# Kernel tuning notes

Measured on AMD Instinct MI355X. Metric: run time of the kernel, lower is better.

## Reference

```python
import jax, jax.numpy as jnp
import numpy as np

N = 50000
E = 800000
HID = 128


def _gat_conv(x, src, dst, W, al, ar, b, n):
    # DGL GATConv, num_heads=1, negative_slope=0.2, bias=True
    z = x @ W                                  # [N, F]
    el = z @ al                                # [N]
    er = z @ ar                                # [N]
    e = jax.nn.leaky_relu(el[src] + er[dst], 0.2)   # [E]
    m = jax.ops.segment_max(e, dst, num_segments=n)  # per-dst max for stable softmax
    ex = jnp.exp(e - m[dst])
    denom = jax.ops.segment_sum(ex, dst, num_segments=n)
    alpha = ex / (denom[dst] + 1e-9)           # edge softmax over incoming edges
    out = jax.ops.segment_sum(alpha[:, None] * z[src], dst, num_segments=n)
    return out + b


def setup_inputs() -> dict:
    key = jax.random.key(0)
    ks = jax.random.split(key, 16)
    inp = {
        "x": jax.random.normal(ks[0], (N, 2), jnp.float32),
        "src": jax.random.randint(ks[1], (E,), 0, N, jnp.int32),
        "dst": jax.random.randint(ks[2], (E,), 0, N, jnp.int32),
        "W1": jax.random.normal(ks[3], (2, HID), jnp.float32) * 0.5,
        "al1": jax.random.normal(ks[4], (HID,), jnp.float32) * 0.1,
        "ar1": jax.random.normal(ks[5], (HID,), jnp.float32) * 0.1,
        "b1": jnp.zeros((HID,), jnp.float32),
        "W2": jax.random.normal(ks[6], (HID, HID), jnp.float32) * (1.0 / np.sqrt(HID)),
        "al2": jax.random.normal(ks[7], (HID,), jnp.float32) * 0.1,
        "ar2": jax.random.normal(ks[8], (HID,), jnp.float32) * 0.1,
        "b2": jnp.zeros((HID,), jnp.float32),
        "Wlin": jax.random.normal(ks[9], (HID, 3), jnp.float32) * (1.0 / np.sqrt(HID)),
        "blin": jnp.zeros((3,), jnp.float32),
        "alpha0": jnp.float32(1.0),
        "beta0": jnp.float32(1.0),
        "gamma0": jnp.float32(1.0),
        "dt": jnp.float32(0.5),
    }
    return inp


def reference(x, src, dst, W1, al1, ar1, b1, W2, al2, ar2, b2, Wlin, blin,
              alpha0, beta0, gamma0, dt):
    h = _gat_conv(x, src, dst, W1, al1, ar1, b1, N)
    h = jax.nn.relu(h)
    h = _gat_conv(h, src, dst, W2, al2, ar2, b2, N)
    h = jax.nn.relu(h)
    h = jax.nn.sigmoid(h @ Wlin + blin)        # [N, 3]
    # (original computes unsplice/splice predictions from alpha0/beta0/gamma0/dt
    #  but does not return them; returned value is the mean over rate channels)
    return h.mean(axis=-1)                     # [N]


if __name__ == "__main__":
    out = reference(**setup_inputs())
    print(out.shape, out.dtype)
```

## Files before the change

### kernel.cpp

```cpp
#include <hip/hip_runtime.h>
#include <math.h>

#define NN 50000
#define EE 800000
#define HIDF 128
#define NPAD 50176

#define BSHIFT 9
#define BKTN 98
#define BCAP 10000

typedef unsigned int uint;
typedef unsigned short ushort;
typedef unsigned char uchar;
typedef short bf16x8 __attribute__((ext_vector_type(8)));
typedef float f32x4 __attribute__((ext_vector_type(4)));

__device__ inline ushort bf16_rtne(float x) {
  uint u = __float_as_uint(x);
  return (ushort)((u + 0x7fffu + ((u >> 16) & 1u)) >> 16);
}
__device__ inline uint pack2_bf16(float a, float b) {
  return (uint)bf16_rtne(a) | ((uint)bf16_rtne(b) << 16);
}
__device__ inline float rdlanef(float p, int jj) {
  return __uint_as_float(__builtin_amdgcn_readlane(__float_as_uint(p), jj));
}

__global__ void k_prep(const float* __restrict__ x, const float* __restrict__ W1,
                       const float* __restrict__ al1, const float* __restrict__ ar1,
                       const float* __restrict__ W2, const float* __restrict__ al2,
                       const float* __restrict__ ar2,
                       ushort* __restrict__ z, float* __restrict__ el, float* __restrict__ er,
                       ushort* __restrict__ Bfrag, float* __restrict__ wel,
                       float* __restrict__ wer, int* __restrict__ bcnt) {
  int b = blockIdx.x, tid = threadIdx.x;
  if (b < 16) {
    int e = b * 1024 + tid * 4;
#pragma unroll
    for (int q = 0; q < 4; ++q, ++e) {
      int k = e >> 7, n = e & 127;
      float v = W2[e];
      ushort hi = bf16_rtne(v);
      ushort lo = bf16_rtne(v - __uint_as_float((uint)hi << 16));
      int g = n >> 4, t = k >> 5;
      int l = (n & 15) | (((k >> 3) & 3) << 4);
      int j = k & 7;
      int idx = ((g * 4 + t) * 64 + l) * 8 + j;
      Bfrag[idx] = hi;
      Bfrag[16384 + idx] = lo;
    }
  } else if (b == 16) {
    if (tid < BKTN) bcnt[tid] = 0;
    if (tid < 128) {
      float acc = 0.f;
      for (int k = 0; k < 128; ++k) acc += W2[k * 128 + tid] * al2[k];
      wel[tid] = acc;
    } else {
      int n = tid - 128;
      float acc = 0.f;
      for (int k = 0; k < 128; ++k) acc += W2[k * 128 + n] * ar2[k];
      wer[n] = acc;
    }
  } else {
    int v = (b - 17) * 4 + (tid >> 6);
    if (v >= NN) return;
    int lane = tid & 63;
    float x0 = x[v * 2 + 0];
    float x1 = x[v * 2 + 1];
    int f0 = lane * 2, f1 = f0 + 1;
    float z0 = fmaf(x0, W1[f0], x1 * W1[HIDF + f0]);
    float z1v = fmaf(x0, W1[f1], x1 * W1[HIDF + f1]);
    ((uint*)(z + (size_t)v * HIDF))[lane] = pack2_bf16(z0, z1v);
    float elp = z0 * al1[f0] + z1v * al1[f1];
    float erp = z0 * ar1[f0] + z1v * ar1[f1];
    for (int o = 32; o; o >>= 1) {
      elp += __shfl_xor(elp, o);
      erp += __shfl_xor(erp, o);
    }
    if (lane == 0) { el[v] = elp; er[v] = erp; }
  }
}

__global__ __launch_bounds__(256) void k_binA(const int* __restrict__ src,
                                              const int* __restrict__ dst,
                                              int* __restrict__ bcnt, uint* __restrict__ bcoo) {
  __shared__ uint stage[4096];
  __shared__ uchar stageb[4096];
  __shared__ int bh[BKTN], bbase[BKTN], gbase[BKTN], lcur[BKTN];
  __shared__ int sc[128];
  int tid = threadIdx.x;
  int e0 = blockIdx.x * 4096;
  int nE = min(4096, EE - e0);
  if (tid < BKTN) bh[tid] = 0;
  __syncthreads();

  int myb[16];
  uint myv[16];
#pragma unroll
  for (int k = 0; k < 16; ++k) {
    int i = e0 + k * 256 + tid;
    myb[k] = -1;
    if (i < EE) {
      int s = src[i], d = dst[i];
      myb[k] = d >> BSHIFT;
      myv[k] = ((uint)s << BSHIFT) | (uint)(d & 511);
      atomicAdd(&bh[myb[k]], 1);
    }
  }
  __syncthreads();

  {
    int v = (tid < BKTN) ? bh[tid] : 0;
    if (tid < 128) sc[tid] = v;
    __syncthreads();
    for (int o = 1; o < 128; o <<= 1) {
      int add = (tid >= o && tid < 128) ? sc[tid - o] : 0;
      __syncthreads();
      if (tid < 128) sc[tid] += add;
      __syncthreads();
    }
    if (tid < BKTN) {
      int excl = sc[tid] - bh[tid];
      bbase[tid] = excl;
      lcur[tid] = excl;
      gbase[tid] = atomicAdd(&bcnt[tid], bh[tid]);
    }
  }
  __syncthreads();

#pragma unroll
  for (int k = 0; k < 16; ++k) {
    if (myb[k] >= 0) {
      int slot = atomicAdd(&lcur[myb[k]], 1);
      stage[slot] = myv[k];
      stageb[slot] = (uchar)myb[k];
    }
  }
  __syncthreads();

  for (int s2 = tid; s2 < nE; s2 += 256) {
    int b = stageb[s2];
    bcoo[(size_t)b * BCAP + gbase[b] + (s2 - bbase[b])] = stage[s2];
  }
}

__global__ __launch_bounds__(256) void k_binB(const uint* __restrict__ bcoo,
                                              const int* __restrict__ bcnt,
                                              int* __restrict__ rowp, int* __restrict__ srcs) {
  __shared__ int h[512], pref[512], ps[256];
  __shared__ int basebuf;
  int b = blockIdx.x, tid = threadIdx.x;
  int cnt = bcnt[b];

  {
    int v = (tid < BKTN) ? bcnt[tid] : 0;
    if (tid < 128) ps[tid] = v;
    __syncthreads();
    for (int o = 1; o < 128; o <<= 1) {
      int add = (tid >= o && tid < 128) ? ps[tid - o] : 0;
      __syncthreads();
      if (tid < 128) ps[tid] += add;
      __syncthreads();
    }
    if (tid == 0) {
      basebuf = (b == 0) ? 0 : ps[b - 1];
      if (b == 0) rowp[NN] = EE;
    }
  }
  h[tid] = 0;
  h[tid + 256] = 0;
  __syncthreads();
  int base = basebuf;
  const uint* mc = bcoo + (size_t)b * BCAP;
  for (int i = tid; i < cnt; i += 256) atomicAdd(&h[mc[i] & 511], 1);
  __syncthreads();
  int a0 = h[2 * tid], a1 = h[2 * tid + 1];
  int s = a0 + a1;
  ps[tid] = s;
  __syncthreads();
  for (int o = 1; o < 256; o <<= 1) {
    int add = (tid >= o) ? ps[tid - o] : 0;
    __syncthreads();
    ps[tid] += add;
    __syncthreads();
  }
  int excl = ps[tid] - s;
  pref[2 * tid] = excl;
  pref[2 * tid + 1] = excl + a0;
  __syncthreads();
  int n0 = b << BSHIFT;
  for (int j = tid; j < 512; j += 256)
    if (n0 + j < NN) rowp[n0 + j] = base + pref[j];
  __syncthreads();
  for (int i = tid; i < cnt; i += 256) {
    uint v = mc[i];
    int pos = atomicAdd(&pref[v & 511], 1);
    srcs[base + pos] = (int)(v >> BSHIFT);
  }
}

__global__ __launch_bounds__(256) void k_gemm_mfma(
    const ushort* __restrict__ Hhi, const ushort* __restrict__ Hlo,
    const ushort* __restrict__ Bfrag, ushort* __restrict__ z) {
  int tid = threadIdx.x;
  int lane = tid & 63;
  int wid = tid >> 6;
  int base = blockIdx.x * 128;

  bf16x8 bhi[2][4], blo[2][4];
  const bf16x8* bp = (const bf16x8*)Bfrag;
#pragma unroll
  for (int gi = 0; gi < 2; ++gi)
#pragma unroll
    for (int t = 0; t < 4; ++t) {
      int idx = ((wid * 2 + gi) * 4 + t) * 64 + lane;
      bhi[gi][t] = bp[idx];
      blo[gi][t] = bp[2048 + idx];
    }

  int arow = lane & 15;
  int koff = (lane >> 4) * 8;
  const bf16x8* ahp = (const bf16x8*)(Hhi + (size_t)(base + arow) * HIDF + koff);
  const bf16x8* alp = (const bf16x8*)(Hlo + (size_t)(base + arow) * HIDF + koff);

  bf16x8 ah[4], av[4];
#pragma unroll
  for (int t = 0; t < 4; ++t) { ah[t] = ahp[t * 4]; av[t] = alp[t * 4]; }

#pragma unroll
  for (int mt = 0; mt < 8; ++mt) {
    bf16x8 nah[4], nav[4];
#pragma unroll
    for (int t = 0; t < 4; ++t) { nah[t] = ah[t]; nav[t] = av[t]; }
    if (mt < 7) {
#pragma unroll
      for (int t = 0; t < 4; ++t) {
        nah[t] = ahp[(mt + 1) * 256 + t * 4];
        nav[t] = alp[(mt + 1) * 256 + t * 4];
      }
    }
    f32x4 c0a = {0.f, 0.f, 0.f, 0.f}, c0b = {0.f, 0.f, 0.f, 0.f};
    f32x4 c1a = {0.f, 0.f, 0.f, 0.f}, c1b = {0.f, 0.f, 0.f, 0.f};
#pragma unroll
    for (int t = 0; t < 4; ++t) {
      f32x4& c0 = (t & 1) ? c0b : c0a;
      f32x4& c1 = (t & 1) ? c1b : c1a;
      c0 = __builtin_amdgcn_mfma_f32_16x16x32_bf16(ah[t], bhi[0][t], c0, 0, 0, 0);
      c1 = __builtin_amdgcn_mfma_f32_16x16x32_bf16(ah[t], bhi[1][t], c1, 0, 0, 0);
      c0 = __builtin_amdgcn_mfma_f32_16x16x32_bf16(ah[t], blo[0][t], c0, 0, 0, 0);
      c1 = __builtin_amdgcn_mfma_f32_16x16x32_bf16(ah[t], blo[1][t], c1, 0, 0, 0);
      c0 = __builtin_amdgcn_mfma_f32_16x16x32_bf16(av[t], bhi[0][t], c0, 0, 0, 0);
      c1 = __builtin_amdgcn_mfma_f32_16x16x32_bf16(av[t], bhi[1][t], c1, 0, 0, 0);
    }
    f32x4 c0 = c0a + c0b;
    f32x4 c1 = c1a + c1b;
    int r0 = base + mt * 16 + (lane >> 4) * 4;
    int cc = wid * 32 + (lane & 15);
    ushort* zp = z + (size_t)r0 * HIDF + cc;
#pragma unroll
    for (int i = 0; i < 4; ++i) {
      zp[i * HIDF] = bf16_rtne(c0[i]);
      zp[i * HIDF + 16] = bf16_rtne(c1[i]);
    }
#pragma unroll
    for (int t = 0; t < 4; ++t) { ah[t] = nah[t]; av[t] = nav[t]; }
  }
}

#define PAIR(JJ)                                                        \
  {                                                                     \
    float pA = rdlanef(p, (JJ)), pB = rdlanef(p, (JJ) + 1);             \
    int sA = __builtin_amdgcn_readlane(s, (JJ));                        \
    int sB = __builtin_amdgcn_readlane(s, (JJ) + 1);                    \
    uint zA = zw[(uint)sA * 64u + (uint)lane];                          \
    uint zB = zw[(uint)sB * 64u + (uint)lane];                          \
    ax = fmaf(pA, __uint_as_float(zA << 16), ax);                       \
    ay = fmaf(pA, __uint_as_float(zA & 0xffff0000u), ay);               \
    ax = fmaf(pB, __uint_as_float(zB << 16), ax);                       \
    ay = fmaf(pB, __uint_as_float(zB & 0xffff0000u), ay);               \
  }

template <int MODE>
__global__ void k_aggregate(const int* __restrict__ rowp, const int* __restrict__ srcs,
                            const float* __restrict__ el, const float* __restrict__ er,
                            const ushort* __restrict__ z, const float* __restrict__ bias,
                            ushort* __restrict__ Hhi, ushort* __restrict__ Hlo,
                            const float* __restrict__ wel, const float* __restrict__ wer,
                            float* __restrict__ elo, float* __restrict__ ero,
                            float* __restrict__ out,
                            const float* __restrict__ Wlin, const float* __restrict__ blin) {
  int v = blockIdx.x * 4 + (threadIdx.x >> 6);
  if (v >= NN) return;
  int lane = threadIdx.x & 63;
  int beg = rowp[v], end = rowp[v + 1];
  float erv = er[v];
  float psum = 0.f;
  float ax = 0.f, ay = 0.f;
  const uint* zw = (const uint*)z;

  for (int cb = beg; cb < end; cb += 64) {
    int j = cb + lane;
    bool valid = j < end;
    int s = srcs[valid ? j : beg];
    float t = el[s] + erv;
    t = fmaxf(t, 0.2f * t);
    float p = valid ? __expf(t) : 0.f;
    psum += p;
    int cnt = min(64, end - cb);
    int bb = 0;
    for (; bb + 16 <= cnt; bb += 16) {
#pragma unroll
      for (int u = 0; u < 16; u += 2) PAIR(bb + u)
    }
    for (; bb < cnt; bb += 2) PAIR(bb)
  }

  float denom = psum;
  for (int o = 32; o; o >>= 1) denom += __shfl_xor(denom, o);
  float inv = 1.0f / (denom + 1e-9f);
  float2 bv = ((const float2*)bias)[lane];
  float ox = fmaxf(fmaf(ax, inv, bv.x), 0.f);
  float oy = fmaxf(fmaf(ay, inv, bv.y), 0.f);

  if (MODE == 1) {
    ushort hx = bf16_rtne(ox), hy = bf16_rtne(oy);
    ((uint*)Hhi)[(size_t)v * 64 + lane] = (uint)hx | ((uint)hy << 16);
    float lx = ox - __uint_as_float((uint)hx << 16);
    float ly = oy - __uint_as_float((uint)hy << 16);
    ((uint*)Hlo)[(size_t)v * 64 + lane] = pack2_bf16(lx, ly);
    float2 wl = ((const float2*)wel)[lane];
    float2 wr = ((const float2*)wer)[lane];
    float ep = ox * wl.x + oy * wl.y;
    float rp = ox * wr.x + oy * wr.y;
    for (int o = 32; o; o >>= 1) {
      ep += __shfl_xor(ep, o);
      rp += __shfl_xor(rp, o);
    }
    if (lane == 0) { elo[v] = ep; ero[v] = rp; }
  } else {
    int f0 = lane * 2;
    const float* w0 = &Wlin[f0 * 3];
    float d0 = fmaf(ox, w0[0], oy * w0[3]);
    float d1 = fmaf(ox, w0[1], oy * w0[4]);
    float d2 = fmaf(ox, w0[2], oy * w0[5]);
    for (int o = 32; o; o >>= 1) {
      d0 += __shfl_xor(d0, o);
      d1 += __shfl_xor(d1, o);
      d2 += __shfl_xor(d2, o);
    }
    if (lane == 0) {
      float s0 = 1.f / (1.f + __expf(-(d0 + blin[0])));
      float s1 = 1.f / (1.f + __expf(-(d1 + blin[1])));
      float s2 = 1.f / (1.f + __expf(-(d2 + blin[2])));
      out[v] = (s0 + s1 + s2) * (1.f / 3.f);
    }
  }
}

extern "C" void kernel_launch(void* const* d_in, const int* in_sizes, int n_in,
                              void* d_out, int out_size, void* d_ws, size_t ws_size,
                              hipStream_t stream) {
  const float* x    = (const float*)d_in[0];
  const int*   src  = (const int*)d_in[1];
  const int*   dst  = (const int*)d_in[2];
  const float* W1   = (const float*)d_in[3];
  const float* al1  = (const float*)d_in[4];
  const float* ar1  = (const float*)d_in[5];
  const float* b1   = (const float*)d_in[6];
  const float* W2   = (const float*)d_in[7];
  const float* al2  = (const float*)d_in[8];
  const float* ar2  = (const float*)d_in[9];
  const float* b2   = (const float*)d_in[10];
  const float* Wlin = (const float*)d_in[11];
  const float* blin = (const float*)d_in[12];
  float* out = (float*)d_out;

  char* ws = (char*)d_ws;
  size_t off = 0;
  auto alloc = [&](size_t bytes) -> char* {
    char* p = ws + off;
    off += (bytes + 255) & ~(size_t)255;
    return p;
  };
  int*    rowp    = (int*)alloc((size_t)(NN + 1) * 4);
  int*    srcs    = (int*)alloc((size_t)EE * 4);
  int*    bcnt    = (int*)alloc(BKTN * 4);
  uint*   bcoo    = (uint*)alloc((size_t)BKTN * BCAP * 4);
  float*  el1     = (float*)alloc((size_t)NN * 4);
  float*  er1     = (float*)alloc((size_t)NN * 4);
  float*  el2     = (float*)alloc((size_t)NN * 4);
  float*  er2     = (float*)alloc((size_t)NN * 4);
  float*  wel     = (float*)alloc(HIDF * 4);
  float*  wer     = (float*)alloc(HIDF * 4);
  ushort* Bfrag   = (ushort*)alloc(2 * 16384 * 2);
  ushort* Z       = (ushort*)alloc((size_t)NPAD * HIDF * 2);
  ushort* Hhi     = (ushort*)alloc((size_t)NPAD * HIDF * 2);
  ushort* Hlo     = (ushort*)alloc((size_t)NPAD * HIDF * 2);

  const int nbNode4 = (NN + 3) / 4;
  const int nbGemm = (NN + 127) / 128;
  const int nbBinA = (EE + 4095) / 4096;

  k_prep<<<17 + nbNode4, 256, 0, stream>>>(x, W1, al1, ar1, W2, al2, ar2,
                                           Z, el1, er1, Bfrag, wel, wer, bcnt);

  k_binA<<<nbBinA, 256, 0, stream>>>(src, dst, bcnt, bcoo);
  k_binB<<<BKTN, 256, 0, stream>>>(bcoo, bcnt, rowp, srcs);

  k_aggregate<1><<<nbNode4, 256, 0, stream>>>(rowp, srcs, el1, er1, Z, b1,
                                              Hhi, Hlo, wel, wer, el2, er2,
                                              nullptr, nullptr, nullptr);

  k_gemm_mfma<<<nbGemm, 256, 0, stream>>>(Hhi, Hlo, Bfrag, Z);
  k_aggregate<2><<<nbNode4, 256, 0, stream>>>(rowp, srcs, el2, er2, Z, b2,
                                              nullptr, nullptr, nullptr, nullptr, nullptr, nullptr,
                                              out, Wlin, blin);
}
```

Measured before the change: 146.3 us.

## Precompute edge exp weights and split aggregation across feature quarters

Adds a per-edge kernel that computes the exponentiated attention logit once and packs it with the source index. Aggregation now launches four blocks per node group, each handling a 32-feature quarter, with four edge subgroups per wave. Partial el2/er2 and final linear outputs are accumulated with atomics, and a separate finalize kernel applies the sigmoid. This raises parallelism and removes readlane serialization, but it adds extra kernels, recomputes the softmax denominator in every quarter, adds atomics, and writes an 8-byte-per-edge array.

```diff
diff --git a/kernel.cpp b/kernel.cpp
--- a/kernel.cpp
+++ b/kernel.cpp
@@ -23,9 +23,8 @@
 __device__ inline uint pack2_bf16(float a, float b) {
   return (uint)bf16_rtne(a) | ((uint)bf16_rtne(b) << 16);
 }
-__device__ inline float rdlanef(float p, int jj) {
-  return __uint_as_float(__builtin_amdgcn_readlane(__float_as_uint(p), jj));
-}
+__device__ inline float lo16(uint z) { return __uint_as_float(z << 16); }
+__device__ inline float hi16(uint z) { return __uint_as_float(z & 0xffff0000u); }
 
 __global__ void k_prep(const float* __restrict__ x, const float* __restrict__ W1,
                        const float* __restrict__ al1, const float* __restrict__ ar1,
@@ -33,7 +32,9 @@
                        const float* __restrict__ ar2,
                        ushort* __restrict__ z, float* __restrict__ el, float* __restrict__ er,
                        ushort* __restrict__ Bfrag, float* __restrict__ wel,
-                       float* __restrict__ wer, int* __restrict__ bcnt) {
+                       float* __restrict__ wer, int* __restrict__ bcnt,
+                       float* __restrict__ el2, float* __restrict__ er2,
+                       float* __restrict__ out3) {
   int b = blockIdx.x, tid = threadIdx.x;
   if (b < 16) {
     int e = b * 1024 + tid * 4;
@@ -78,7 +79,11 @@
       elp += __shfl_xor(elp, o);
       erp += __shfl_xor(erp, o);
     }
-    if (lane == 0) { el[v] = elp; er[v] = erp; }
+    if (lane == 0) {
+      el[v] = elp; er[v] = erp;
+      el2[v] = 0.f; er2[v] = 0.f;
+      out3[v] = 0.f; out3[NN + v] = 0.f; out3[2 * NN + v] = 0.f;
+    }
   }
 }
 
@@ -147,7 +152,8 @@
 
 __global__ __launch_bounds__(256) void k_binB(const uint* __restrict__ bcoo,
                                               const int* __restrict__ bcnt,
-                                              int* __restrict__ rowp, int* __restrict__ srcs) {
+                                              int* __restrict__ rowp, int* __restrict__ srcs,
+                                              int* __restrict__ dstc) {
   __shared__ int h[512], pref[512], ps[256];
   __shared__ int basebuf;
   int b = blockIdx.x, tid = threadIdx.x;
@@ -197,7 +203,19 @@
     uint v = mc[i];
     int pos = atomicAdd(&pref[v & 511], 1);
     srcs[base + pos] = (int)(v >> BSHIFT);
-  }
+    dstc[base + pos] = n0 + (int)(v & 511);
+  }
+}
+
+__global__ void k_edgep(const int* __restrict__ srcs, const int* __restrict__ dstc,
+                        const float* __restrict__ el, const float* __restrict__ er,
+                        uint2* __restrict__ e2) {
+  int j = blockIdx.x * 256 + threadIdx.x;
+  if (j >= EE) return;
+  int s = srcs[j];
+  float t = el[s] + er[dstc[j]];
+  t = fmaxf(t, 0.2f * t);
+  e2[j] = make_uint2((uint)s, __float_as_uint(__expf(t)));
 }
 
 __global__ __launch_bounds__(256) void k_gemm_mfma(
@@ -268,94 +286,107 @@
   }
 }
 
-#define PAIR(JJ)                                                        \
-  {                                                                     \
-    float pA = rdlanef(p, (JJ)), pB = rdlanef(p, (JJ) + 1);             \
-    int sA = __builtin_amdgcn_readlane(s, (JJ));                        \
-    int sB = __builtin_amdgcn_readlane(s, (JJ) + 1);                    \
-    uint zA = zw[(uint)sA * 64u + (uint)lane];                          \
-    uint zB = zw[(uint)sB * 64u + (uint)lane];                          \
-    ax = fmaf(pA, __uint_as_float(zA << 16), ax);                       \
-    ay = fmaf(pA, __uint_as_float(zA & 0xffff0000u), ay);               \
-    ax = fmaf(pB, __uint_as_float(zB << 16), ax);                       \
-    ay = fmaf(pB, __uint_as_float(zB & 0xffff0000u), ay);               \
-  }
-
 template <int MODE>
-__global__ void k_aggregate(const int* __restrict__ rowp, const int* __restrict__ srcs,
-                            const float* __restrict__ el, const float* __restrict__ er,
-                            const ushort* __restrict__ z, const float* __restrict__ bias,
-                            ushort* __restrict__ Hhi, ushort* __restrict__ Hlo,
-                            const float* __restrict__ wel, const float* __restrict__ wer,
-                            float* __restrict__ elo, float* __restrict__ ero,
-                            float* __restrict__ out,
-                            const float* __restrict__ Wlin, const float* __restrict__ blin) {
-  int v = blockIdx.x * 4 + (threadIdx.x >> 6);
+__global__ __launch_bounds__(256) void k_aggq(
+    const int* __restrict__ rowp, const uint2* __restrict__ e2,
+    const ushort* __restrict__ z, const float* __restrict__ bias,
+    ushort* __restrict__ Hhi, ushort* __restrict__ Hlo,
+    const float* __restrict__ wel, const float* __restrict__ wer,
+    float* __restrict__ el2, float* __restrict__ er2,
+    float* __restrict__ out3) {
+  int bid = blockIdx.x;
+  int q = bid & 3;
+  int v = (bid >> 2) * 4 + (threadIdx.x >> 6);
   if (v >= NN) return;
   int lane = threadIdx.x & 63;
+  int g = lane >> 4, li = lane & 15;
   int beg = rowp[v], end = rowp[v + 1];
-  float erv = er[v];
-  float psum = 0.f;
-  float ax = 0.f, ay = 0.f;
   const uint* zw = (const uint*)z;
-
+  uint qoff = (uint)(q * 16 + li);
+
+  float ps = 0.f;
   for (int cb = beg; cb < end; cb += 64) {
     int j = cb + lane;
+    if (j < end) ps += __uint_as_float(e2[j].y);
+  }
+  for (int o = 32; o; o >>= 1) ps += __shfl_xor(ps, o);
+
+  float a0 = 0.f, a1 = 0.f;
+  int jj = beg;
+  for (; jj + 8 <= end; jj += 8) {
+    uint2 eA = e2[jj + g];
+    uint2 eB = e2[jj + 4 + g];
+    uint zA = zw[eA.x * 64u + qoff];
+    uint zB = zw[eB.x * 64u + qoff];
+    float pA = __uint_as_float(eA.y), pB = __uint_as_float(eB.y);
+    a0 = fmaf(pA, lo16(zA), a0);
+    a1 = fmaf(pA, hi16(zA), a1);
+    a0 = fmaf(pB, lo16(zB), a0);
+    a1 = fmaf(pB, hi16(zB), a1);
+  }
+  for (; jj < end; jj += 4) {
+    int j = jj + g;
     bool valid = j < end;
-    int s = srcs[valid ? j : beg];
-    float t = el[s] + erv;
-    t = fmaxf(t, 0.2f * t);
-    float p = valid ? __expf(t) : 0.f;
-    psum += p;
-    int cnt = min(64, end - cb);
-    int bb = 0;
-    for (; bb + 16 <= cnt; bb += 16) {
-#pragma unroll
-      for (int u = 0; u < 16; u += 2) PAIR(bb + u)
-    }
-    for (; bb < cnt; bb += 2) PAIR(bb)
-  }
-
-  float denom = psum;
-  for (int o = 32; o; o >>= 1) denom += __shfl_xor(denom, o);
-  float inv = 1.0f / (denom + 1e-9f);
-  float2 bv = ((const float2*)bias)[lane];
-  float ox = fmaxf(fmaf(ax, inv, bv.x), 0.f);
-  float oy = fmaxf(fmaf(ay, inv, bv.y), 0.f);
+    uint2 eA = e2[valid ? j : beg];
+    float pA = valid ? __uint_as_float(eA.y) : 0.f;
+    uint zA = zw[eA.x * 64u + qoff];
+    a0 = fmaf(pA, lo16(zA), a0);
+    a1 = fmaf(pA, hi16(zA), a1);
+  }
+  a0 += __shfl_xor(a0, 16);
+  a0 += __shfl_xor(a0, 32);
+  a1 += __shfl_xor(a1, 16);
+  a1 += __shfl_xor(a1, 32);
+
+  float inv = 1.0f / (ps + 1e-9f);
+  int f0 = q * 32 + li * 2;
+  float ox = fmaxf(fmaf(a0, inv, bias[f0]), 0.f);
+  float oy = fmaxf(fmaf(a1, inv, bias[f0 + 1]), 0.f);
+
+  if (lane >= 16) return;
 
   if (MODE == 1) {
     ushort hx = bf16_rtne(ox), hy = bf16_rtne(oy);
-    ((uint*)Hhi)[(size_t)v * 64 + lane] = (uint)hx | ((uint)hy << 16);
+    ((uint*)Hhi)[(size_t)v * 64 + qoff] = (uint)hx | ((uint)hy << 16);
     float lx = ox - __uint_as_float((uint)hx << 16);
     float ly = oy - __uint_as_float((uint)hy << 16);
-    ((uint*)Hlo)[(size_t)v * 64 + lane] = pack2_bf16(lx, ly);
-    float2 wl = ((const float2*)wel)[lane];
-    float2 wr = ((const float2*)wer)[lane];
-    float ep = ox * wl.x + oy * wl.y;
-    float rp = ox * wr.x + oy * wr.y;
-    for (int o = 32; o; o >>= 1) {
+    ((uint*)Hlo)[(size_t)v * 64 + qoff] = pack2_bf16(lx, ly);
+    float ep = ox * wel[f0] + oy * wel[f0 + 1];
+    float rp = ox * wer[f0] + oy * wer[f0 + 1];
+    for (int o = 8; o; o >>= 1) {
       ep += __shfl_xor(ep, o);
       rp += __shfl_xor(rp, o);
     }
-    if (lane == 0) { elo[v] = ep; ero[v] = rp; }
+    if (li == 0) {
+      atomicAdd(&el2[v], ep);
+      atomicAdd(&er2[v], rp);
+    }
   } else {
-    int f0 = lane * 2;
-    const float* w0 = &Wlin[f0 * 3];
-    float d0 = fmaf(ox, w0[0], oy * w0[3]);
-    float d1 = fmaf(ox, w0[1], oy * w0[4]);
-    float d2 = fmaf(ox, w0[2], oy * w0[5]);
-    for (int o = 32; o; o >>= 1) {
+    const float* wr = wel + f0 * 3;
+    float d0 = ox * wr[0] + oy * wr[3];
+    float d1 = ox * wr[1] + oy * wr[4];
+    float d2 = ox * wr[2] + oy * wr[5];
+    for (int o = 8; o; o >>= 1) {
       d0 += __shfl_xor(d0, o);
       d1 += __shfl_xor(d1, o);
       d2 += __shfl_xor(d2, o);
     }
-    if (lane == 0) {
-      float s0 = 1.f / (1.f + __expf(-(d0 + blin[0])));
-      float s1 = 1.f / (1.f + __expf(-(d1 + blin[1])));
-      float s2 = 1.f / (1.f + __expf(-(d2 + blin[2])));
-      out[v] = (s0 + s1 + s2) * (1.f / 3.f);
-    }
-  }
+    if (li == 0) {
+      atomicAdd(&out3[v], d0);
+      atomicAdd(&out3[NN + v], d1);
+      atomicAdd(&out3[2 * NN + v], d2);
+    }
+  }
+}
+
+__global__ void k_final(const float* __restrict__ out3, const float* __restrict__ blin,
+                        float* __restrict__ out) {
+  int v = blockIdx.x * 256 + threadIdx.x;
+  if (v >= NN) return;
+  float s0 = 1.f / (1.f + __expf(-(out3[v] + blin[0])));
+  float s1 = 1.f / (1.f + __expf(-(out3[NN + v] + blin[1])));
+  float s2 = 1.f / (1.f + __expf(-(out3[2 * NN + v] + blin[2])));
+  out[v] = (s0 + s1 + s2) * (1.f / 3.f);
 }
 
 extern "C" void kernel_launch(void* const* d_in, const int* in_sizes, int n_in,
@@ -383,37 +414,45 @@
     off += (bytes + 255) & ~(size_t)255;
     return p;
   };
-  int*    rowp    = (int*)alloc((size_t)(NN + 1) * 4);
-  int*    srcs    = (int*)alloc((size_t)EE * 4);
-  int*    bcnt    = (int*)alloc(BKTN * 4);
-  uint*   bcoo    = (uint*)alloc((size_t)BKTN * BCAP * 4);
-  float*  el1     = (float*)alloc((size_t)NN * 4);
-  float*  er1     = (float*)alloc((size_t)NN * 4);
-  float*  el2     = (float*)alloc((size_t)NN * 4);
-  float*  er2     = (float*)alloc((size_t)NN * 4);
-  float*  wel     = (float*)alloc(HIDF * 4);
-  float*  wer     = (float*)alloc(HIDF * 4);
-  ushort* Bfrag   = (ushort*)alloc(2 * 16384 * 2);
-  ushort* Z       = (ushort*)alloc((size_t)NPAD * HIDF * 2);
-  ushort* Hhi     = (ushort*)alloc((size_t)NPAD * HIDF * 2);
-  ushort* Hlo     = (ushort*)alloc((size_t)NPAD * HIDF * 2);
+  int*    rowp  = (int*)alloc((size_t)(NN + 1) * 4);
+  int*    srcs  = (int*)alloc((size_t)EE * 4);
+  int*    dstc  = (int*)alloc((size_t)EE * 4);
+  uint2*  e2    = (uint2*)alloc((size_t)EE * 8);
+  int*    bcnt  = (int*)alloc(BKTN * 4);
+  uint*   bcoo  = (uint*)alloc((size_t)BKTN * BCAP * 4);
+  float*  el1   = (float*)alloc((size_t)NN * 4);
+  float*  er1   = (float*)alloc((size_t)NN * 4);
+  float*  el2   = (float*)alloc((size_t)NN * 4);
+  float*  er2   = (float*)alloc((size_t)NN * 4);
+  float*  out3  = (float*)alloc((size_t)NN * 3 * 4);
+  float*  wel   = (float*)alloc(HIDF * 4);
+  float*  wer   = (float*)alloc(HIDF * 4);
+  ushort* Bfrag = (ushort*)alloc(2 * 16384 * 2);
+  ushort* Z     = (ushort*)alloc((size_t)NPAD * HIDF * 2);
+  ushort* Hhi   = (ushort*)alloc((size_t)NPAD * HIDF * 2);
+  ushort* Hlo   = (ushort*)alloc((size_t)NPAD * HIDF * 2);
 
   const int nbNode4 = (NN + 3) / 4;
+  const int nbAggQ = nbNode4 * 4;
   const int nbGemm = (NN + 127) / 128;
   const int nbBinA = (EE + 4095) / 4096;
+  const int nbEdge = (EE + 255) / 256;
+  const int nbN = (NN + 255) / 256;
 
   k_prep<<<17 + nbNode4, 256, 0, stream>>>(x, W1, al1, ar1, W2, al2, ar2,
-                                           Z, el1, er1, Bfrag, wel, wer, bcnt);
+                                           Z, el1, er1, Bfrag, wel, wer, bcnt,
+                                           el2, er2, out3);
 
   k_binA<<<nbBinA, 256, 0, stream>>>(src, dst, bcnt, bcoo);
-  k_binB<<<BKTN, 256, 0, stream>>>(bcoo, bcnt, rowp, srcs);
-
-  k_aggregate<1><<<nbNode4, 256, 0, stream>>>(rowp, srcs, el1, er1, Z, b1,
-                                              Hhi, Hlo, wel, wer, el2, er2,
-                                              nullptr, nullptr, nullptr);
+  k_binB<<<BKTN, 256, 0, stream>>>(bcoo, bcnt, rowp, srcs, dstc);
+
+  k_edgep<<<nbEdge, 256, 0, stream>>>(srcs, dstc, el1, er1, e2);
+  k_aggq<1><<<nbAggQ, 256, 0, stream>>>(rowp, e2, Z, b1, Hhi, Hlo, wel, wer,
+                                        el2, er2, nullptr);
 
   k_gemm_mfma<<<nbGemm, 256, 0, stream>>>(Hhi, Hlo, Bfrag, Z);
-  k_aggregate<2><<<nbNode4, 256, 0, stream>>>(rowp, srcs, el2, er2, Z, b2,
-                                              nullptr, nullptr, nullptr, nullptr, nullptr, nullptr,
-                                              out, Wlin, blin);
-}
+  k_edgep<<<nbEdge, 256, 0, stream>>>(srcs, dstc, el2, er2, e2);
+  k_aggq<2><<<nbAggQ, 256, 0, stream>>>(rowp, e2, Z, b2, nullptr, nullptr, Wlin, nullptr,
+                                        nullptr, nullptr, out3);
+  k_final<<<nbN, 256, 0, stream>>>(out3, blin, out);
+}
```

Result: slower. 319.5 us (+118.4%).
